# Optimization experiments

Hardware: AMD Instinct MI355X
Metric: run time of the kernel (lower is better)

## Reference

```python
import jax, jax.numpy as jnp
import numpy as np

D_MODEL = 1024
NHEAD = 16
HEAD_DIM = D_MODEL // NHEAD
MAX_DIST = 128


def setup_inputs() -> dict:
    key = jax.random.key(0)
    ks = jax.random.split(key, 6)
    B, T = 2, 2048
    x = jax.random.normal(ks[0], (B, T, D_MODEL), dtype=jnp.float32)
    Wqkv = jax.random.normal(ks[1], (D_MODEL, 3 * D_MODEL), dtype=jnp.float32) * 0.02
    bqkv = jnp.zeros((3 * D_MODEL,), dtype=jnp.float32)
    Wout = jax.random.normal(ks[2], (D_MODEL, D_MODEL), dtype=jnp.float32) * 0.02
    bout = jnp.zeros((D_MODEL,), dtype=jnp.float32)
    rel_emb = jax.random.normal(ks[3], (2 * MAX_DIST + 1, NHEAD), dtype=jnp.float32) * 0.02
    return {"x": x, "Wqkv": Wqkv, "bqkv": bqkv, "Wout": Wout, "bout": bout, "rel_emb": rel_emb}


def _rel_bias(rel_emb, seq_len):
    pos = jnp.arange(seq_len)
    rel = pos[None, :] - pos[:, None]                       # [S,S]
    rel = jnp.clip(rel, -MAX_DIST, MAX_DIST) + MAX_DIST
    bias = rel_emb[rel]                                     # [S,S,H]
    bias = jnp.transpose(bias, (2, 0, 1))                   # [H,S,S]
    causal_mask = jnp.triu(jnp.ones((seq_len, seq_len), dtype=bool), k=1)
    return jnp.where(causal_mask[None, :, :], -jnp.inf, bias)


def reference(x, Wqkv, bqkv, Wout, bout, rel_emb):
    B, T, C = x.shape
    qkv = x @ Wqkv + bqkv                                   # [B,T,3C]
    q, k, v = jnp.split(qkv, 3, axis=-1)

    def split_heads(t):
        return jnp.transpose(t.reshape(B, T, NHEAD, HEAD_DIM), (0, 2, 1, 3))  # [B,H,T,Dh]

    q, k, v = split_heads(q), split_heads(k), split_heads(v)
    scale = jnp.sqrt(jnp.float32(HEAD_DIM))
    attn = jnp.einsum('bhtd,bhsd->bhts', q, k) / scale      # [B,H,T,S]
    bias = _rel_bias(rel_emb, T)                            # [H,T,S] (causal -inf mask baked in)
    attn = attn + bias[None, :, :, :]
    attn = jax.nn.softmax(attn, axis=-1)
    out = jnp.einsum('bhts,bhsd->bhtd', attn, v)            # [B,H,T,Dh]
    out = jnp.transpose(out, (0, 2, 1, 3)).reshape(B, T, C)
    return out @ Wout + bout
```

## Files before the change

### kernel.cpp

```cpp
#include <hip/hip_runtime.h>
#include <hip/hip_bf16.h>

typedef __attribute__((ext_vector_type(8))) short s8v;
typedef __attribute__((ext_vector_type(4))) float f4v;

__device__ __forceinline__ ushort f2bf(float f) {
    union { float f; unsigned u; } cv; cv.f = f;
    unsigned u = cv.u;
    unsigned lsb = (u >> 16) & 1u;
    u += 0x7fffu + lsb;
    return (ushort)(u >> 16);
}

typedef __attribute__((address_space(1))) void gvoid;
typedef __attribute__((address_space(3))) void lvoid;
__device__ __forceinline__ void gl_lds16(const ushort* g, ushort* l) {
    __builtin_amdgcn_global_load_lds((gvoid*)g, (lvoid*)l, 16, 0, 0);
}

__global__ void cast_bf16_kernel(const float* __restrict__ in, ushort* __restrict__ out, int n4) {
    int i = blockIdx.x * blockDim.x + threadIdx.x;
    if (i >= n4) return;
    float4 v = reinterpret_cast<const float4*>(in)[i];
    ushort4 o;
    o.x = f2bf(v.x); o.y = f2bf(v.y); o.z = f2bf(v.z); o.w = f2bf(v.w);
    reinterpret_cast<ushort4*>(out)[i] = o;
}

__global__ void transpose_cast_kernel(const float* __restrict__ in, ushort* __restrict__ out,
                                      int R, int C) {
    __shared__ float tile[32][33];
    int c0 = blockIdx.x * 32, r0 = blockIdx.y * 32;
    int tx = threadIdx.x & 31, ty = threadIdx.x >> 5;
    #pragma unroll
    for (int i = 0; i < 32; i += 8)
        tile[ty + i][tx] = in[(size_t)(r0 + ty + i) * C + c0 + tx];
    __syncthreads();
    #pragma unroll
    for (int i = 0; i < 32; i += 8)
        out[(size_t)(c0 + ty + i) * R + r0 + tx] = f2bf(tile[tx][ty + i]);
}

__global__ __launch_bounds__(256) void vtrans_kernel(
    const ushort* __restrict__ qkv, ushort* __restrict__ vt_g, int T)
{
    __shared__ ushort tile[64][72];
    const int sb = blockIdx.x * 64, bh = blockIdx.y;
    const int b = bh >> 4, h = bh & 15;
    const int t = threadIdx.x;
    const int r0 = t >> 3, c0 = (t & 7) * 8;
    const ushort* vsrc = qkv + (size_t)b * T * 3072 + 2048 + h * 64;
    *(s8v*)&tile[r0][c0]      = *(const s8v*)(vsrc + (size_t)(sb + r0) * 3072 + c0);
    *(s8v*)&tile[32 + r0][c0] = *(const s8v*)(vsrc + (size_t)(sb + 32 + r0) * 3072 + c0);
    __syncthreads();
    ushort* vdst = vt_g + (size_t)bh * 64 * T;
    s8v o0, o1;
    #pragma unroll
    for (int j = 0; j < 8; j++) {
        o0[j] = (short)tile[c0 + j][r0];
        o1[j] = (short)tile[c0 + j][32 + r0];
    }
    *(s8v*)(vdst + (size_t)r0 * T + sb + c0)        = o0;
    *(s8v*)(vdst + (size_t)(32 + r0) * T + sb + c0) = o1;
}

template <bool OUT_BF16>
__global__ __launch_bounds__(256) void gemm_bt_kernel(
    const ushort* __restrict__ A, const ushort* __restrict__ Bt,
    const float* __restrict__ bias, void* __restrict__ Cout,
    int M, int N, int K)
{
    __shared__ ushort As[128][64];
    __shared__ ushort Bs[128][64];
    const int t = threadIdx.x;
    const int m0 = blockIdx.y * 128, n0 = blockIdx.x * 128;
    const int wave = t >> 6, lane = t & 63;
    const int lr = lane & 15, lg = lane >> 4;
    const int wm = (wave >> 1) * 64, wn = (wave & 1) * 64;
    const int lrow = lane >> 3;
    const int lcol = (lane & 7) * 8;

    f4v acc[4][4];
    #pragma unroll
    for (int i = 0; i < 4; i++)
        #pragma unroll
        for (int j = 0; j < 4; j++)
            acc[i][j] = (f4v){0.f, 0.f, 0.f, 0.f};

    for (int k0 = 0; k0 < K; k0 += 64) {
        __syncthreads();
        #pragma unroll
        for (int i = 0; i < 4; i++) {
            int j = wave * 4 + i;
            int row = j * 8 + lrow;
            gl_lds16(A  + (size_t)(m0 + row) * K + k0 + lcol, &As[j * 8][0]);
            gl_lds16(Bt + (size_t)(n0 + row) * K + k0 + lcol, &Bs[j * 8][0]);
        }
        __syncthreads();
        #pragma unroll
        for (int ks = 0; ks < 64; ks += 32) {
            s8v af[4], bfr[4];
            #pragma unroll
            for (int mb = 0; mb < 4; mb++)
                af[mb] = *reinterpret_cast<const s8v*>(&As[wm + mb * 16 + lr][ks + lg * 8]);
            #pragma unroll
            for (int nb = 0; nb < 4; nb++)
                bfr[nb] = *reinterpret_cast<const s8v*>(&Bs[wn + nb * 16 + lr][ks + lg * 8]);
            #pragma unroll
            for (int mb = 0; mb < 4; mb++)
                #pragma unroll
                for (int nb = 0; nb < 4; nb++)
                    acc[mb][nb] = __builtin_amdgcn_mfma_f32_16x16x32_bf16(af[mb], bfr[nb], acc[mb][nb], 0, 0, 0);
        }
    }

    #pragma unroll
    for (int mb = 0; mb < 4; mb++) {
        #pragma unroll
        for (int nb = 0; nb < 4; nb++) {
            int col = n0 + wn + nb * 16 + lr;
            float bv = bias[col];
            #pragma unroll
            for (int r = 0; r < 4; r++) {
                int row = m0 + wm + mb * 16 + lg * 4 + r;
                float val = acc[mb][nb][r] + bv;
                if (OUT_BF16)
                    reinterpret_cast<ushort*>(Cout)[(size_t)row * N + col] = f2bf(val);
                else
                    reinterpret_cast<float*>(Cout)[(size_t)row * N + col] = val;
            }
        }
    }
}

__device__ __forceinline__ void attn_tile(
    const s8v qf0, const s8v qf1, int qb, int sb,
    int wave, int lr, int lg,
    const ushort (*Ks)[72], const ushort (*Vs)[72],
    ushort (*pw)[72],
    const float* rel_lds,
    float* m_r, float* l_r, f4v* o_acc)
{
    f4v sacc[4];
    #pragma unroll
    for (int cb = 0; cb < 4; cb++) {
        sacc[cb] = (f4v){0.f, 0.f, 0.f, 0.f};
        s8v kf0 = *(const s8v*)&Ks[cb * 16 + lr][lg * 8];
        s8v kf1 = *(const s8v*)&Ks[cb * 16 + lr][32 + lg * 8];
        sacc[cb] = __builtin_amdgcn_mfma_f32_16x16x32_bf16(qf0, kf0, sacc[cb], 0, 0, 0);
        sacc[cb] = __builtin_amdgcn_mfma_f32_16x16x32_bf16(qf1, kf1, sacc[cb], 0, 0, 0);
    }

    if (sb + 192 <= qb) {
        float c = rel_lds[0];
        #pragma unroll
        for (int cb = 0; cb < 4; cb++)
            #pragma unroll
            for (int r = 0; r < 4; r++)
                sacc[cb][r] = sacc[cb][r] * 0.125f + c;
    } else {
        #pragma unroll
        for (int cb = 0; cb < 4; cb++) {
            int s = sb + cb * 16 + lr;
            #pragma unroll
            for (int r = 0; r < 4; r++) {
                int q = qb + wave * 16 + lg * 4 + r;
                int rel = s - q;
                rel = (rel < -128 ? -128 : (rel > 128 ? 128 : rel)) + 128;
                float val = sacc[cb][r] * 0.125f + rel_lds[rel];
                if (s > q) val = -3.0e38f;
                sacc[cb][r] = val;
            }
        }
    }

    #pragma unroll
    for (int r = 0; r < 4; r++) {
        float mx = fmaxf(fmaxf(sacc[0][r], sacc[1][r]), fmaxf(sacc[2][r], sacc[3][r]));
        #pragma unroll
        for (int off = 1; off < 16; off <<= 1)
            mx = fmaxf(mx, __shfl_xor(mx, off, 64));
        float mnew = fmaxf(m_r[r], mx);
        float alpha = exp2f((m_r[r] - mnew) * 1.44269504f);
        m_r[r] = mnew;
        l_r[r] *= alpha;
        #pragma unroll
        for (int d = 0; d < 4; d++) o_acc[d][r] *= alpha;
        float sum = 0.f;
        #pragma unroll
        for (int cb = 0; cb < 4; cb++) {
            float p = exp2f((sacc[cb][r] - mnew) * 1.44269504f);
            sacc[cb][r] = p;
            sum += p;
        }
        #pragma unroll
        for (int off = 1; off < 16; off <<= 1)
            sum += __shfl_xor(sum, off, 64);
        l_r[r] += sum;
    }

    #pragma unroll
    for (int cb = 0; cb < 4; cb++)
        #pragma unroll
        for (int r = 0; r < 4; r++)
            pw[lg * 4 + r][cb * 16 + lr] = f2bf(sacc[cb][r]);

    #pragma unroll
    for (int ch = 0; ch < 2; ch++) {
        s8v pf = *(const s8v*)&pw[lr][ch * 32 + lg * 8];
        #pragma unroll
        for (int d = 0; d < 4; d++) {
            s8v vf = *(const s8v*)&Vs[d * 16 + lr][ch * 32 + lg * 8];
            o_acc[d] = __builtin_amdgcn_mfma_f32_16x16x32_bf16(pf, vf, o_acc[d], 0, 0, 0);
        }
    }
}

__global__ __launch_bounds__(256, 2) void attn_kernel(
    const ushort* __restrict__ qkv, const ushort* __restrict__ vt_g,
    const float* __restrict__ rel_emb, ushort* __restrict__ attn_out, int T)
{
    __shared__ ushort Ks[64][72];
    __shared__ ushort Vs[64][72];
    __shared__ ushort p_lds[4][16][72];
    __shared__ float rel_lds[257];

    const int t = threadIdx.x;
    const int nQ = T / 64;
    const int lo = blockIdx.x;
    const int hi = nQ - 1 - lo;
    const int qbL = lo * 64, qbH = hi * 64;
    const int bh = blockIdx.y;
    const int b = bh >> 4, h = bh & 15;
    const size_t rowb = (size_t)b * T;

    for (int i = t; i < 257; i += 256) rel_lds[i] = rel_emb[i * 16 + h];

    const int wave = t >> 6, lane = t & 63;
    const int lr = lane & 15, lg = lane >> 4;
    const int sr = t >> 3, sc = (t & 7) * 8;

    const ushort* kbase = qkv + rowb * 3072 + 1024 + h * 64;
    const ushort* vbase = vt_g + (size_t)bh * 64 * T;

    const ushort* qptrL = qkv + (rowb + qbL + wave * 16 + lr) * 3072 + h * 64;
    s8v qL0 = *(const s8v*)(qptrL + lg * 8);
    s8v qL1 = *(const s8v*)(qptrL + 32 + lg * 8);
    const ushort* qptrH = qkv + (rowb + qbH + wave * 16 + lr) * 3072 + h * 64;
    s8v qH0 = *(const s8v*)(qptrH + lg * 8);
    s8v qH1 = *(const s8v*)(qptrH + 32 + lg * 8);

    float mL[4], lL[4], mH[4], lH[4];
    f4v oL[4], oH[4];
    #pragma unroll
    for (int r = 0; r < 4; r++) { mL[r] = -3.0e38f; lL[r] = 0.f; mH[r] = -3.0e38f; lH[r] = 0.f; }
    #pragma unroll
    for (int d = 0; d < 4; d++) { oL[d] = (f4v){0.f,0.f,0.f,0.f}; oH[d] = (f4v){0.f,0.f,0.f,0.f}; }

    const int nt = hi + 1;

    s8v ka0 = *(const s8v*)(kbase + (size_t)sr * 3072 + sc);
    s8v ka1 = *(const s8v*)(kbase + (size_t)(32 + sr) * 3072 + sc);
    s8v va0 = *(const s8v*)(vbase + (size_t)sr * T + sc);
    s8v va1 = *(const s8v*)(vbase + (size_t)(32 + sr) * T + sc);

    for (int st = 0; st < nt; ++st) {
        const int sb = st * 64;
        __syncthreads();
        *(s8v*)&Ks[sr][sc]      = ka0;
        *(s8v*)&Ks[32 + sr][sc] = ka1;
        *(s8v*)&Vs[sr][sc]      = va0;
        *(s8v*)&Vs[32 + sr][sc] = va1;
        __syncthreads();

        if (st + 1 < nt) {
            const int sn = sb + 64;
            ka0 = *(const s8v*)(kbase + (size_t)(sn + sr) * 3072 + sc);
            ka1 = *(const s8v*)(kbase + (size_t)(sn + 32 + sr) * 3072 + sc);
            va0 = *(const s8v*)(vbase + (size_t)sr * T + sn + sc);
            va1 = *(const s8v*)(vbase + (size_t)(32 + sr) * T + sn + sc);
        }

        attn_tile(qH0, qH1, qbH, sb, wave, lr, lg, Ks, Vs, p_lds[wave], rel_lds, mH, lH, oH);
        if (st <= lo)
            attn_tile(qL0, qL1, qbL, sb, wave, lr, lg, Ks, Vs, p_lds[wave], rel_lds, mL, lL, oL);
    }

    #pragma unroll
    for (int r = 0; r < 4; r++) {
        float invH = 1.0f / lH[r];
        float invL = 1.0f / lL[r];
        int rowH = qbH + wave * 16 + lg * 4 + r;
        int rowL = qbL + wave * 16 + lg * 4 + r;
        #pragma unroll
        for (int d = 0; d < 4; d++) {
            attn_out[(rowb + rowH) * 1024 + h * 64 + d * 16 + lr] = f2bf(oH[d][r] * invH);
            attn_out[(rowb + rowL) * 1024 + h * 64 + d * 16 + lr] = f2bf(oL[d][r] * invL);
        }
    }
}

extern "C" void kernel_launch(void* const* d_in, const int* in_sizes, int n_in,
                              void* d_out, int out_size, void* d_ws, size_t ws_size,
                              hipStream_t stream) {
    const float* x       = (const float*)d_in[0];
    const float* Wqkv    = (const float*)d_in[1];
    const float* bqkv    = (const float*)d_in[2];
    const float* Wout    = (const float*)d_in[3];
    const float* bout    = (const float*)d_in[4];
    const float* rel_emb = (const float*)d_in[5];
    float* out = (float*)d_out;

    const int M = in_sizes[0] / 1024;
    const int T = 2048;
    const int B = M / T;

    ushort* x_bf = (ushort*)d_ws;
    ushort* Wq_t = x_bf + (size_t)M * 1024;
    ushort* Wo_t = Wq_t + (size_t)3072 * 1024;
    ushort* qkv  = Wo_t + (size_t)1024 * 1024;
    ushort* attn = qkv + (size_t)M * 3072;
    ushort* vt_g = attn + (size_t)M * 1024;

    hipLaunchKernelGGL(cast_bf16_kernel, dim3((M * 1024 / 4 + 255) / 256), dim3(256), 0, stream,
                       x, x_bf, M * 1024 / 4);
    hipLaunchKernelGGL(transpose_cast_kernel, dim3(3072 / 32, 1024 / 32), dim3(256), 0, stream,
                       Wqkv, Wq_t, 1024, 3072);
    hipLaunchKernelGGL(transpose_cast_kernel, dim3(1024 / 32, 1024 / 32), dim3(256), 0, stream,
                       Wout, Wo_t, 1024, 1024);
    hipLaunchKernelGGL((gemm_bt_kernel<true>), dim3(3072 / 128, M / 128), dim3(256), 0, stream,
                       x_bf, Wq_t, bqkv, (void*)qkv, M, 3072, 1024);
    hipLaunchKernelGGL(vtrans_kernel, dim3(T / 64, B * 16), dim3(256), 0, stream,
                       qkv, vt_g, T);
    hipLaunchKernelGGL(attn_kernel, dim3((T / 64) / 2, B * 16), dim3(256), 0, stream,
                       qkv, vt_g, rel_emb, attn, T);
    hipLaunchKernelGGL((gemm_bt_kernel<false>), dim3(1024 / 128, M / 128), dim3(256), 0, stream,
                       attn, Wo_t, bout, (void*)out, M, 1024, 1024);
}
```

Measured before the change: 249.0 us.

## Transpose attention MFMA layout so each lane owns one query row with lazy rescale

Swaps the MFMA operand order so the score and output tiles are transposed: each lane holds a single query row. Row max and sum then need only two cross-lane shuffles instead of four per row. Also folds log2(e) into the scale and the relative-bias table, skips rescaling the accumulator unless the max grows by more than 8 (in log2 units), raises wave priority around the MFMA blocks, and writes P and the output through packed 64-bit LDS stores with vectorized global stores. The lazy rescale lets unnormalized values grow up to about 2^8, which relies on fp32 headroom and bf16 P precision. Staging the output through LDS adds a shared-memory round trip per wave.

Result: faster. 225.2 us (-9.6%).

```diff
diff --git a/kernel.cpp b/kernel.cpp
--- a/kernel.cpp
+++ b/kernel.cpp
@@ -133,23 +133,26 @@
     }
 }
 
-__device__ __forceinline__ void attn_tile(
-    const s8v qf0, const s8v qf1, int qb, int sb,
-    int wave, int lr, int lg,
+__device__ __forceinline__ void attn_tile_sw(
+    const s8v qf0, const s8v qf1, int q_abs, int qb, int sb,
+    int lr, int lg,
     const ushort (*Ks)[72], const ushort (*Vs)[72],
-    ushort (*pw)[72],
+    ushort (*pT)[72],
     const float* rel_lds,
-    float* m_r, float* l_r, f4v* o_acc)
-{
+    float& m, float& l, f4v* oT)
+{
+    const float SC = 0.125f * 1.44269504f;
     f4v sacc[4];
+    __builtin_amdgcn_s_setprio(1);
     #pragma unroll
     for (int cb = 0; cb < 4; cb++) {
         sacc[cb] = (f4v){0.f, 0.f, 0.f, 0.f};
         s8v kf0 = *(const s8v*)&Ks[cb * 16 + lr][lg * 8];
         s8v kf1 = *(const s8v*)&Ks[cb * 16 + lr][32 + lg * 8];
-        sacc[cb] = __builtin_amdgcn_mfma_f32_16x16x32_bf16(qf0, kf0, sacc[cb], 0, 0, 0);
-        sacc[cb] = __builtin_amdgcn_mfma_f32_16x16x32_bf16(qf1, kf1, sacc[cb], 0, 0, 0);
-    }
+        sacc[cb] = __builtin_amdgcn_mfma_f32_16x16x32_bf16(kf0, qf0, sacc[cb], 0, 0, 0);
+        sacc[cb] = __builtin_amdgcn_mfma_f32_16x16x32_bf16(kf1, qf1, sacc[cb], 0, 0, 0);
+    }
+    __builtin_amdgcn_s_setprio(0);
 
     if (sb + 192 <= qb) {
         float c = rel_lds[0];
@@ -157,63 +160,95 @@
         for (int cb = 0; cb < 4; cb++)
             #pragma unroll
             for (int r = 0; r < 4; r++)
-                sacc[cb][r] = sacc[cb][r] * 0.125f + c;
+                sacc[cb][r] = sacc[cb][r] * SC + c;
     } else {
         #pragma unroll
         for (int cb = 0; cb < 4; cb++) {
-            int s = sb + cb * 16 + lr;
             #pragma unroll
             for (int r = 0; r < 4; r++) {
-                int q = qb + wave * 16 + lg * 4 + r;
-                int rel = s - q;
+                int s = sb + cb * 16 + lg * 4 + r;
+                int rel = s - q_abs;
                 rel = (rel < -128 ? -128 : (rel > 128 ? 128 : rel)) + 128;
-                float val = sacc[cb][r] * 0.125f + rel_lds[rel];
-                if (s > q) val = -3.0e38f;
+                float val = sacc[cb][r] * SC + rel_lds[rel];
+                if (s > q_abs) val = -3.0e38f;
                 sacc[cb][r] = val;
             }
         }
     }
 
-    #pragma unroll
-    for (int r = 0; r < 4; r++) {
-        float mx = fmaxf(fmaxf(sacc[0][r], sacc[1][r]), fmaxf(sacc[2][r], sacc[3][r]));
-        #pragma unroll
-        for (int off = 1; off < 16; off <<= 1)
-            mx = fmaxf(mx, __shfl_xor(mx, off, 64));
-        float mnew = fmaxf(m_r[r], mx);
-        float alpha = exp2f((m_r[r] - mnew) * 1.44269504f);
-        m_r[r] = mnew;
-        l_r[r] *= alpha;
-        #pragma unroll
-        for (int d = 0; d < 4; d++) o_acc[d][r] *= alpha;
-        float sum = 0.f;
-        #pragma unroll
-        for (int cb = 0; cb < 4; cb++) {
-            float p = exp2f((sacc[cb][r] - mnew) * 1.44269504f);
+    float pm0 = fmaxf(fmaxf(sacc[0][0], sacc[0][1]), fmaxf(sacc[0][2], sacc[0][3]));
+    float pm1 = fmaxf(fmaxf(sacc[1][0], sacc[1][1]), fmaxf(sacc[1][2], sacc[1][3]));
+    float pm2 = fmaxf(fmaxf(sacc[2][0], sacc[2][1]), fmaxf(sacc[2][2], sacc[2][3]));
+    float pm3 = fmaxf(fmaxf(sacc[3][0], sacc[3][1]), fmaxf(sacc[3][2], sacc[3][3]));
+    float pm = fmaxf(fmaxf(pm0, pm1), fmaxf(pm2, pm3));
+    pm = fmaxf(pm, __shfl_xor(pm, 16, 64));
+    pm = fmaxf(pm, __shfl_xor(pm, 32, 64));
+
+    if (__any(pm > m + 8.0f)) {
+        float mnew = fmaxf(m, pm);
+        float alpha = exp2f(m - mnew);
+        l *= alpha;
+        #pragma unroll
+        for (int d = 0; d < 4; d++)
+            #pragma unroll
+            for (int r = 0; r < 4; r++)
+                oT[d][r] *= alpha;
+        m = mnew;
+    }
+
+    float sum = 0.f;
+    #pragma unroll
+    for (int cb = 0; cb < 4; cb++) {
+        #pragma unroll
+        for (int r = 0; r < 4; r++) {
+            float p = exp2f(sacc[cb][r] - m);
             sacc[cb][r] = p;
             sum += p;
         }
-        #pragma unroll
-        for (int off = 1; off < 16; off <<= 1)
-            sum += __shfl_xor(sum, off, 64);
-        l_r[r] += sum;
-    }
-
-    #pragma unroll
-    for (int cb = 0; cb < 4; cb++)
-        #pragma unroll
-        for (int r = 0; r < 4; r++)
-            pw[lg * 4 + r][cb * 16 + lr] = f2bf(sacc[cb][r]);
-
+    }
+    sum += __shfl_xor(sum, 16, 64);
+    sum += __shfl_xor(sum, 32, 64);
+    l += sum;
+
+    #pragma unroll
+    for (int cb = 0; cb < 4; cb++) {
+        unsigned lo = (unsigned)f2bf(sacc[cb][0]) | ((unsigned)f2bf(sacc[cb][1]) << 16);
+        unsigned hi = (unsigned)f2bf(sacc[cb][2]) | ((unsigned)f2bf(sacc[cb][3]) << 16);
+        *(unsigned long long*)&pT[lr][cb * 16 + lg * 4] =
+            (unsigned long long)lo | ((unsigned long long)hi << 32);
+    }
+
+    __builtin_amdgcn_s_setprio(1);
     #pragma unroll
     for (int ch = 0; ch < 2; ch++) {
-        s8v pf = *(const s8v*)&pw[lr][ch * 32 + lg * 8];
+        s8v pf = *(const s8v*)&pT[lr][ch * 32 + lg * 8];
         #pragma unroll
         for (int d = 0; d < 4; d++) {
             s8v vf = *(const s8v*)&Vs[d * 16 + lr][ch * 32 + lg * 8];
-            o_acc[d] = __builtin_amdgcn_mfma_f32_16x16x32_bf16(pf, vf, o_acc[d], 0, 0, 0);
-        }
-    }
+            oT[d] = __builtin_amdgcn_mfma_f32_16x16x32_bf16(vf, pf, oT[d], 0, 0, 0);
+        }
+    }
+    __builtin_amdgcn_s_setprio(0);
+}
+
+__device__ __forceinline__ void store_O(
+    f4v* oT, float l, int lr, int lg, int lane, int wave,
+    ushort (*pT)[72], int qb, size_t rowb, int h, ushort* __restrict__ attn_out)
+{
+    float inv = 1.0f / l;
+    #pragma unroll
+    for (int d = 0; d < 4; d++) {
+        unsigned lo = (unsigned)f2bf(oT[d][0] * inv) | ((unsigned)f2bf(oT[d][1] * inv) << 16);
+        unsigned hi = (unsigned)f2bf(oT[d][2] * inv) | ((unsigned)f2bf(oT[d][3] * inv) << 16);
+        *(unsigned long long*)&pT[lr][d * 16 + lg * 4] =
+            (unsigned long long)lo | ((unsigned long long)hi << 32);
+    }
+    int q_r = lane >> 2, part = lane & 3;
+    s8v a = *(const s8v*)&pT[q_r][part * 16];
+    s8v b = *(const s8v*)&pT[q_r][part * 16 + 8];
+    ushort* dst = attn_out + (rowb + qb + wave * 16 + q_r) * 1024 + h * 64 + part * 16;
+    *(s8v*)dst = a;
+    *(s8v*)(dst + 8) = b;
 }
 
 __global__ __launch_bounds__(256, 2) void attn_kernel(
@@ -234,7 +269,7 @@
     const int b = bh >> 4, h = bh & 15;
     const size_t rowb = (size_t)b * T;
 
-    for (int i = t; i < 257; i += 256) rel_lds[i] = rel_emb[i * 16 + h];
+    for (int i = t; i < 257; i += 256) rel_lds[i] = rel_emb[i * 16 + h] * 1.44269504f;
 
     const int wave = t >> 6, lane = t & 63;
     const int lr = lane & 15, lg = lane >> 4;
@@ -243,17 +278,17 @@
     const ushort* kbase = qkv + rowb * 3072 + 1024 + h * 64;
     const ushort* vbase = vt_g + (size_t)bh * 64 * T;
 
-    const ushort* qptrL = qkv + (rowb + qbL + wave * 16 + lr) * 3072 + h * 64;
+    const int qaL = qbL + wave * 16 + lr;
+    const int qaH = qbH + wave * 16 + lr;
+    const ushort* qptrL = qkv + (rowb + qaL) * 3072 + h * 64;
     s8v qL0 = *(const s8v*)(qptrL + lg * 8);
     s8v qL1 = *(const s8v*)(qptrL + 32 + lg * 8);
-    const ushort* qptrH = qkv + (rowb + qbH + wave * 16 + lr) * 3072 + h * 64;
+    const ushort* qptrH = qkv + (rowb + qaH) * 3072 + h * 64;
     s8v qH0 = *(const s8v*)(qptrH + lg * 8);
     s8v qH1 = *(const s8v*)(qptrH + 32 + lg * 8);
 
-    float mL[4], lL[4], mH[4], lH[4];
+    float mL = -3.0e38f, lL = 0.f, mH = -3.0e38f, lH = 0.f;
     f4v oL[4], oH[4];
-    #pragma unroll
-    for (int r = 0; r < 4; r++) { mL[r] = -3.0e38f; lL[r] = 0.f; mH[r] = -3.0e38f; lH[r] = 0.f; }
     #pragma unroll
     for (int d = 0; d < 4; d++) { oL[d] = (f4v){0.f,0.f,0.f,0.f}; oH[d] = (f4v){0.f,0.f,0.f,0.f}; }
 
@@ -281,23 +316,13 @@
             va1 = *(const s8v*)(vbase + (size_t)(32 + sr) * T + sn + sc);
         }
 
-        attn_tile(qH0, qH1, qbH, sb, wave, lr, lg, Ks, Vs, p_lds[wave], rel_lds, mH, lH, oH);
+        attn_tile_sw(qH0, qH1, qaH, qbH, sb, lr, lg, Ks, Vs, p_lds[wave], rel_lds, mH, lH, oH);
         if (st <= lo)
-            attn_tile(qL0, qL1, qbL, sb, wave, lr, lg, Ks, Vs, p_lds[wave], rel_lds, mL, lL, oL);
-    }
-
-    #pragma unroll
-    for (int r = 0; r < 4; r++) {
-        float invH = 1.0f / lH[r];
-        float invL = 1.0f / lL[r];
-        int rowH = qbH + wave * 16 + lg * 4 + r;
-        int rowL = qbL + wave * 16 + lg * 4 + r;
-        #pragma unroll
-        for (int d = 0; d < 4; d++) {
-            attn_out[(rowb + rowH) * 1024 + h * 64 + d * 16 + lr] = f2bf(oH[d][r] * invH);
-            attn_out[(rowb + rowL) * 1024 + h * 64 + d * 16 + lr] = f2bf(oL[d][r] * invL);
-        }
-    }
+            attn_tile_sw(qL0, qL1, qaL, qbL, sb, lr, lg, Ks, Vs, p_lds[wave], rel_lds, mL, lL, oL);
+    }
+
+    store_O(oH, lH, lr, lg, lane, wave, p_lds[wave], qbH, rowb, h, attn_out);
+    store_O(oL, lL, lr, lg, lane, wave, p_lds[wave], qbL, rowb, h, attn_out);
 }
 
 extern "C" void kernel_launch(void* const* d_in, const int* in_sizes, int n_in,
```
